# Kernel tuning notes

Hardware: AMD Instinct MI355X
Metric: run time of the kernel (lower is better)

The kernel has to match this reference:

```python
import jax, jax.numpy as jnp
import numpy as np

HEADS = 8
DIM_HEAD = 64
ROT_DIM = DIM_HEAD // 2  # RotaryEmbedding(dim=head_dim//2) rotates first 32 dims of each head
THETA = 10000.0


def _rope_cos_sin(T, dtype):
    # rotary_embedding_torch: freqs = 1/theta**(arange(0,dim,2)/dim), len dim//2,
    # angles repeated interleaved across pairs -> (T, ROT_DIM)
    inv = 1.0 / (THETA ** (jnp.arange(0, ROT_DIM, 2, dtype=jnp.float32) / ROT_DIM))
    ang = jnp.arange(T, dtype=jnp.float32)[:, None] * inv[None, :]      # (T, ROT_DIM/2)
    ang = jnp.repeat(ang, 2, axis=-1)                                   # (T, ROT_DIM) interleaved
    return jnp.cos(ang).astype(dtype), jnp.sin(ang).astype(dtype)


def _rotate_half(x):
    # pairs (x1, x2) -> (-x2, x1), interleaved layout '... (d 2)'
    x = x.reshape(x.shape[:-1] + (-1, 2))
    x = jnp.stack([-x[..., 1], x[..., 0]], axis=-1)
    return x.reshape(x.shape[:-2] + (-1,))


def _apply_rope(x, cos, sin):
    # x: (N, h, T, dh); rotate first ROT_DIM dims, pass through the rest
    xr, xp = x[..., :ROT_DIM], x[..., ROT_DIM:]
    xr = xr * cos[None, None, :, :] + _rotate_half(xr) * sin[None, None, :, :]
    return jnp.concatenate([xr, xp], axis=-1)


def setup_inputs() -> dict:
    key = jax.random.key(0)
    k1, k2, k3 = jax.random.split(key, 3)
    B, T, H, W, D = 2, 32, 32, 32, 512
    inner = HEADS * DIM_HEAD
    x = jax.random.normal(k1, (B, T, H, W, D), dtype=jnp.float32)
    w_qkv = jax.random.normal(k2, (D, 3 * inner), dtype=jnp.float32) * (D ** -0.5)
    w_out = jax.random.normal(k3, (inner, D), dtype=jnp.float32) * (inner ** -0.5)
    b_out = jnp.zeros((D,), dtype=jnp.float32)
    return {"x": x, "w_qkv": w_qkv, "w_out": w_out, "b_out": b_out}


def reference(x, w_qkv, w_out, b_out):
    B, T, H, W, D = x.shape
    qkv = jnp.einsum('bthwd,de->bthwe', x, w_qkv)               # (B,T,H,W,3*inner)
    q, k, v = jnp.split(qkv, 3, axis=-1)

    def to_axial(t):  # (B,T,H,W,inner) -> (B*H*W, heads, T, dh)
        t = t.reshape(B, T, H, W, HEADS, DIM_HEAD)
        t = jnp.transpose(t, (0, 2, 3, 4, 1, 5))
        return t.reshape(B * H * W, HEADS, T, DIM_HEAD)

    q, k, v = to_axial(q), to_axial(k), to_axial(v)
    cos, sin = _rope_cos_sin(T, x.dtype)
    q = _apply_rope(q, cos, sin)
    k = _apply_rope(k, cos, sin)

    scale = DIM_HEAD ** -0.5
    scores = jnp.einsum('nhqd,nhkd->nhqk', q, k) * scale        # (N,h,T,T)
    causal = jnp.tril(jnp.ones((T, T), dtype=bool))
    scores = jnp.where(causal[None, None, :, :], scores, jnp.finfo(scores.dtype).min)
    attn = jax.nn.softmax(scores, axis=-1)
    out = jnp.einsum('nhqk,nhkd->nhqd', attn, v)                # (N,h,T,dh)

    out = out.reshape(B, H, W, HEADS, T, DIM_HEAD)
    out = jnp.transpose(out, (0, 4, 1, 2, 3, 5)).reshape(B, T, H, W, HEADS * DIM_HEAD)
    return jnp.einsum('bthwe,ed->bthwd', out, w_out) + b_out
```

## Files before the change

### kernel.cpp

```cpp
#include <hip/hip_runtime.h>
#include <hip/hip_bf16.h>
#include <math.h>

#define HEADS  8
#define TT     32
#define DMODEL 512
#define HWSZ   1024
#define TSTRIDE (HWSZ*DMODEL)

#define NQKV (3*DMODEL*DMODEL)
#define NOUT (DMODEL*DMODEL)
#define NTAB 512

typedef __attribute__((ext_vector_type(8)))  short bf16x8;
typedef __attribute__((ext_vector_type(16))) float f32x16;
typedef __attribute__((ext_vector_type(4)))  short s16x4;
typedef __attribute__((ext_vector_type(2)))  unsigned int u32x2;

__device__ __forceinline__ unsigned short f2bf(float f) {
    unsigned int u = __builtin_bit_cast(unsigned int, f);
    u += 0x7FFFu + ((u >> 16) & 1u);
    return (unsigned short)(u >> 16);
}

__device__ __forceinline__ unsigned int pk_bf(float a, float b) {
    return (unsigned int)f2bf(a) | ((unsigned int)f2bf(b) << 16);
}

__device__ __forceinline__ f32x16 fz16() {
    f32x16 v = {0.f,0.f,0.f,0.f,0.f,0.f,0.f,0.f,0.f,0.f,0.f,0.f,0.f,0.f,0.f,0.f};
    return v;
}

__global__ __launch_bounds__(256)
void taa_prep(const float* __restrict__ wqkv, const float* __restrict__ wout,
              unsigned short* __restrict__ ws) {
    long i = (long)blockIdx.x * 256 + threadIdx.x;
    unsigned short* wqf = ws;
    unsigned short* wof = ws + NQKV;
    float* cs = (float*)(wof + NOUT);
    float* sn = cs + NTAB;
    if (i < NQKV) {
        int i8 = (int)(i & 7), lane = (int)((i >> 3) & 63), blk = (int)(i >> 9);
        int k05 = blk & 15, t = blk >> 4;
        int n = t * 16 + (lane & 15);
        int k = k05 * 32 + (lane >> 4) * 8 + i8;
        wqf[i] = f2bf(wqkv[(long)k * 1536 + n]);
    } else if (i < NQKV + NOUT) {
        long j = i - NQKV;
        int i8 = (int)(j & 7), lane = (int)((j >> 3) & 63), blk = (int)(j >> 9);
        int k05 = blk & 15, t = blk >> 4;
        int col = t * 16 + (lane & 15);
        int k = k05 * 32 + (lane >> 4) * 8 + i8;
        wof[j] = f2bf(wout[(long)k * 512 + col]);
    } else if (i < NQKV + NOUT + NTAB) {
        int j = (int)(i - NQKV - NOUT);
        int t = j >> 4, f = j & 15;
        float inv = powf(10000.f, -(float)(2 * f) / 32.f);
        float sv, cv;
        sincosf((float)t * inv, &sv, &cv);
        cs[j] = cv; sn[j] = sv;
    }
}

#define X_OFF  0
#define Q_OFF  65536
#define K_OFF  81920
#define V_OFF  98304
#define PV_OFF 114688
#define CS_OFF 131072
#define SN_OFF 133120
#define LDS_SZ 135168

#define XF(g, blk, ln) (X_OFF + ((g) << 15) + ((blk) << 10) + ((((ln) << 4)) ^ (((blk) & 7) << 4)))
#define RS(base, r, cB) ((base) + ((r) << 7) + ((cB) ^ (((r) & 7) << 4)))
#define VS(base, d, cB) ((base) + ((d) << 6) + ((cB) ^ (((d) & 7) << 3)))

#define MFMA16(a, b, c) __builtin_amdgcn_mfma_f32_16x16x32_bf16((a), (b), (c), 0, 0, 0)
#define MFMA32(a, b, c) __builtin_amdgcn_mfma_f32_32x32x16_bf16((a), (b), (c), 0, 0, 0)

__global__ __launch_bounds__(512, 1)
void taa_main(const float* __restrict__ x,
              const unsigned short* __restrict__ ws,
              const float* __restrict__ b_out,
              float* __restrict__ out) {
    extern __shared__ __align__(16) unsigned char smem[];

    const unsigned short* wqf = ws;
    const unsigned short* wof = ws + NQKV;
    const float* cs_gl = (const float*)(wof + NOUT);
    const float* sn_gl = cs_gl + NTAB;

    const int tid  = threadIdx.x;
    const int lane = tid & 63;
    const int wv   = tid >> 6;
    const int quad = lane >> 4;
    const int lid  = lane & 15;

    const int n0 = blockIdx.x * 2;
    const long long base0 = ((long long)(n0 >> 10) * (TT * HWSZ) + (n0 & 1023)) * DMODEL;
    const int n1 = n0 + 1;
    const long long base1 = ((long long)(n1 >> 10) * (TT * HWSZ) + (n1 & 1023)) * DMODEL;

    float* cs_l = (float*)(smem + CS_OFF);
    float* sn_l = (float*)(smem + SN_OFF);
    for (int i = tid; i < NTAB; i += 512) { cs_l[i] = cs_gl[i]; sn_l[i] = sn_gl[i]; }

    for (int idx = tid; idx < 4096; idx += 512) {
        int g  = idx >> 11;
        int r  = (idx >> 6) & 31;
        int c8 = idx & 63;
        long long bg = g ? base1 : base0;
        const float4* src = (const float4*)(x + bg + (long long)r * TSTRIDE + c8 * 8);
        float4 f0 = src[0], f1 = src[1];
        s16x4 lo, hi;
        lo[0] = (short)f2bf(f0.x); lo[1] = (short)f2bf(f0.y);
        lo[2] = (short)f2bf(f0.z); lo[3] = (short)f2bf(f0.w);
        hi[0] = (short)f2bf(f1.x); hi[1] = (short)f2bf(f1.y);
        hi[2] = (short)f2bf(f1.z); hi[3] = (short)f2bf(f1.w);
        int blk = ((r >> 4) << 4) + (c8 >> 2);
        int ln  = ((c8 & 3) << 4) | (r & 15);
        int dest = XF(g, blk, ln);
        *(s16x4*)(smem + dest)     = lo;
        *(s16x4*)(smem + dest + 8) = hi;
    }

    typedef __attribute__((ext_vector_type(4))) float f32x4;
    f32x4 oacc[4][2][2];
    #pragma unroll
    for (int j = 0; j < 4; ++j)
        #pragma unroll
        for (int g = 0; g < 2; ++g)
            #pragma unroll
            for (int mt = 0; mt < 2; ++mt) oacc[j][g][mt] = (f32x4){0.f, 0.f, 0.f, 0.f};

    __syncthreads();

    for (int it = 0; it < 4; ++it) {
        const int hpair = it * 2;

        for (int rnd = 0; rnd < 3; ++rnd) {
            int ct  = rnd * 8 + wv;
            int m   = ct >> 3;
            int hh  = (ct >> 2) & 1;
            int t16 = ct & 3;
            int T   = m * 32 + (hpair + hh) * 4 + t16;
            const unsigned short* wp = wqf + ((long)T * 16) * 512 + lane * 8;
            f32x4 acc[2][2];
            #pragma unroll
            for (int g = 0; g < 2; ++g)
                #pragma unroll
                for (int mt = 0; mt < 2; ++mt) acc[g][mt] = (f32x4){0.f, 0.f, 0.f, 0.f};
            #pragma unroll 4
            for (int k05 = 0; k05 < 16; ++k05) {
                bf16x8 bw = *(const bf16x8*)(wp + (long)k05 * 512);
                #pragma unroll
                for (int g = 0; g < 2; ++g)
                    #pragma unroll
                    for (int mt = 0; mt < 2; ++mt) {
                        bf16x8 a = *(const bf16x8*)(smem + XF(g, mt * 16 + k05, lane));
                        acc[g][mt] = MFMA16(a, bw, acc[g][mt]);
                    }
            }
            if (m < 2) {
                int dstb = ((m == 0) ? Q_OFF : K_OFF) + hh * 4096;
                if (t16 < 2) {
                    #pragma unroll
                    for (int g = 0; g < 2; ++g)
                        #pragma unroll
                        for (int mt = 0; mt < 2; ++mt)
                            #pragma unroll
                            for (int r = 0; r < 4; ++r) {
                                float v = acc[g][mt][r];
                                float p = __shfl_xor(v, 1, 64);
                                int trow = mt * 16 + quad * 4 + r;
                                int colh = t16 * 16 + lid;
                                int jj = colh >> 1;
                                float cv = cs_l[trow * 16 + jj];
                                float sv = sn_l[trow * 16 + jj];
                                float res = (colh & 1) ? (v * cv + p * sv) : (v * cv - p * sv);
                                *(unsigned short*)(smem + RS(dstb + g * 8192, trow, colh * 2)) = f2bf(res);
                            }
                } else {
                    #pragma unroll
                    for (int g = 0; g < 2; ++g)
                        #pragma unroll
                        for (int mt = 0; mt < 2; ++mt)
                            #pragma unroll
                            for (int r = 0; r < 4; ++r) {
                                int trow = mt * 16 + quad * 4 + r;
                                *(unsigned short*)(smem + RS(dstb + g * 8192, trow, (t16 * 16 + lid) * 2)) = f2bf(acc[g][mt][r]);
                            }
                }
            } else {
                #pragma unroll
                for (int g = 0; g < 2; ++g)
                    #pragma unroll
                    for (int mt = 0; mt < 2; ++mt) {
                        int d  = t16 * 16 + lid;
                        int t0 = mt * 16 + quad * 4;
                        s16x4 pk;
                        pk[0] = (short)f2bf(acc[g][mt][0]); pk[1] = (short)f2bf(acc[g][mt][1]);
                        pk[2] = (short)f2bf(acc[g][mt][2]); pk[3] = (short)f2bf(acc[g][mt][3]);
                        *(s16x4*)(smem + VS(V_OFF + (g * 2 + hh) * 4096, d, t0 * 2)) = pk;
                    }
            }
        }
        __syncthreads();

        {
            int g  = wv >> 2;
            int hh = (wv >> 1) & 1;
            int dt = wv & 1;
            int qr  = Q_OFF  + (g * 2 + hh) * 4096;
            int kr  = K_OFF  + (g * 2 + hh) * 4096;
            int vr  = V_OFF  + (g * 2 + hh) * 4096;
            int pvr = PV_OFF + (g * 2 + hh) * 4096;
            int tq = lane & 31;
            int hf = lane >> 5;

            f32x16 sc = fz16();
            #pragma unroll
            for (int j = 0; j < 4; ++j) {
                bf16x8 aK = *(const bf16x8*)(smem + RS(kr, tq, j * 32 + hf * 16));
                bf16x8 bQ = *(const bf16x8*)(smem + RS(qr, tq, j * 32 + hf * 16));
                sc = MFMA32(aK, bQ, sc);
            }
            float pe[16];
            float mx = -1e30f;
            #pragma unroll
            for (int r = 0; r < 16; ++r) {
                int tk = (r & 3) + 8 * (r >> 2) + 4 * hf;
                float v = (tk <= tq) ? sc[r] * 0.125f : -1e30f;
                pe[r] = v;
                mx = fmaxf(mx, v);
            }
            mx = fmaxf(mx, __shfl_xor(mx, 32, 64));
            float sum = 0.f;
            #pragma unroll
            for (int r = 0; r < 16; ++r) {
                float e = __expf(pe[r] - mx);
                pe[r] = e;
                sum += e;
            }
            sum += __shfl_xor(sum, 32, 64);
            float inv = 1.f / sum;
            bf16x8 pa0, pa1;
            #pragma unroll
            for (int i2 = 0; i2 < 8; ++i2) {
                pa0[i2] = (short)f2bf(pe[i2] * inv);
                pa1[i2] = (short)f2bf(pe[8 + i2] * inv);
            }
            int d = dt * 32 + tq;
            f32x16 o = fz16();
            {
                s16x4 lo = *(const s16x4*)(smem + VS(vr, d, 8 * hf));
                s16x4 hi = *(const s16x4*)(smem + VS(vr, d, 16 + 8 * hf));
                bf16x8 bv;
                bv[0] = lo[0]; bv[1] = lo[1]; bv[2] = lo[2]; bv[3] = lo[3];
                bv[4] = hi[0]; bv[5] = hi[1]; bv[6] = hi[2]; bv[7] = hi[3];
                o = MFMA32(bv, pa0, o);
            }
            {
                s16x4 lo = *(const s16x4*)(smem + VS(vr, d, 32 + 8 * hf));
                s16x4 hi = *(const s16x4*)(smem + VS(vr, d, 48 + 8 * hf));
                bf16x8 bv;
                bv[0] = lo[0]; bv[1] = lo[1]; bv[2] = lo[2]; bv[3] = lo[3];
                bv[4] = hi[0]; bv[5] = hi[1]; bv[6] = hi[2]; bv[7] = hi[3];
                o = MFMA32(bv, pa1, o);
            }
            #pragma unroll
            for (int c = 0; c < 4; ++c) {
                u32x2 pk2;
                pk2[0] = pk_bf(o[4 * c + 0], o[4 * c + 1]);
                pk2[1] = pk_bf(o[4 * c + 2], o[4 * c + 3]);
                int db = dt * 32 + c * 8 + 4 * hf;
                *(u32x2*)(smem + RS(pvr, tq, db * 2)) = pk2;
            }
        }
        __syncthreads();

        {
            #pragma unroll
            for (int k05h = 0; k05h < 4; ++k05h) {
                int hh   = k05h >> 1;
                int dblk = k05h & 1;
                int kb   = (hpair + hh) * 2 + dblk;
                bf16x8 a[2][2];
                #pragma unroll
                for (int g = 0; g < 2; ++g)
                    #pragma unroll
                    for (int mt = 0; mt < 2; ++mt)
                        a[g][mt] = *(const bf16x8*)(smem + RS(PV_OFF + (g * 2 + hh) * 4096, lid + 16 * mt, dblk * 64 + quad * 16));
                #pragma unroll
                for (int j = 0; j < 4; ++j) {
                    int ct = wv + 8 * j;
                    bf16x8 bw = *(const bf16x8*)(wof + ((long)(ct * 16 + kb)) * 512 + lane * 8);
                    #pragma unroll
                    for (int g = 0; g < 2; ++g)
                        #pragma unroll
                        for (int mt = 0; mt < 2; ++mt)
                            oacc[j][g][mt] = MFMA16(a[g][mt], bw, oacc[j][g][mt]);
                }
            }
        }
    }

    #pragma unroll
    for (int j = 0; j < 4; ++j) {
        int col = (wv + 8 * j) * 16 + lid;
        float bias = b_out[col];
        #pragma unroll
        for (int g = 0; g < 2; ++g) {
            long long bg = g ? base1 : base0;
            #pragma unroll
            for (int mt = 0; mt < 2; ++mt)
                #pragma unroll
                for (int r = 0; r < 4; ++r) {
                    int t = mt * 16 + quad * 4 + r;
                    out[bg + (long long)t * TSTRIDE + col] = oacc[j][g][mt][r] + bias;
                }
        }
    }
}

extern "C" void kernel_launch(void* const* d_in, const int* in_sizes, int n_in,
                              void* d_out, int out_size, void* d_ws, size_t ws_size,
                              hipStream_t stream) {
    const float* x     = (const float*)d_in[0];
    const float* w_qkv = (const float*)d_in[1];
    const float* w_out = (const float*)d_in[2];
    const float* b_out = (const float*)d_in[3];
    float* out = (float*)d_out;
    (void)in_sizes; (void)n_in; (void)out_size; (void)ws_size;

    unsigned short* ws = (unsigned short*)d_ws;

    taa_prep<<<dim3(4098), dim3(256), 0, stream>>>(w_qkv, w_out, ws);
    taa_main<<<dim3(1024), dim3(512), LDS_SZ, stream>>>(x, ws, b_out, out);
}
```

Baseline: 228.8 us.

## Process one axial sequence per block with 256 threads instead of two

Each block now handles a single (b,h,w) sequence with 4 waves instead of two sequences with 8 waves. This halves LDS use (about 68KB) and drops the launch bound minimum, so two blocks can reside per CU and the grid doubles to 2048. In exchange, each weight tile loaded from global memory is reused across only one sequence instead of two, which doubles weight traffic per output.

```diff
diff --git a/kernel.cpp b/kernel.cpp
--- a/kernel.cpp
+++ b/kernel.cpp
@@ -64,22 +64,22 @@
 }
 
 #define X_OFF  0
-#define Q_OFF  65536
-#define K_OFF  81920
-#define V_OFF  98304
-#define PV_OFF 114688
-#define CS_OFF 131072
-#define SN_OFF 133120
-#define LDS_SZ 135168
-
-#define XF(g, blk, ln) (X_OFF + ((g) << 15) + ((blk) << 10) + ((((ln) << 4)) ^ (((blk) & 7) << 4)))
+#define Q_OFF  32768
+#define K_OFF  40960
+#define V_OFF  49152
+#define PV_OFF 57344
+#define CS_OFF 65536
+#define SN_OFF 67584
+#define LDS_SZ 69632
+
+#define XF(blk, ln) (X_OFF + ((blk) << 10) + ((((ln) << 4)) ^ (((blk) & 7) << 4)))
 #define RS(base, r, cB) ((base) + ((r) << 7) + ((cB) ^ (((r) & 7) << 4)))
 #define VS(base, d, cB) ((base) + ((d) << 6) + ((cB) ^ (((d) & 7) << 3)))
 
 #define MFMA16(a, b, c) __builtin_amdgcn_mfma_f32_16x16x32_bf16((a), (b), (c), 0, 0, 0)
 #define MFMA32(a, b, c) __builtin_amdgcn_mfma_f32_32x32x16_bf16((a), (b), (c), 0, 0, 0)
 
-__global__ __launch_bounds__(512, 1)
+__global__ __launch_bounds__(256)
 void taa_main(const float* __restrict__ x,
               const unsigned short* __restrict__ ws,
               const float* __restrict__ b_out,
@@ -97,21 +97,17 @@
     const int quad = lane >> 4;
     const int lid  = lane & 15;
 
-    const int n0 = blockIdx.x * 2;
-    const long long base0 = ((long long)(n0 >> 10) * (TT * HWSZ) + (n0 & 1023)) * DMODEL;
-    const int n1 = n0 + 1;
-    const long long base1 = ((long long)(n1 >> 10) * (TT * HWSZ) + (n1 & 1023)) * DMODEL;
+    const int n  = blockIdx.x;
+    const long long base = ((long long)(n >> 10) * (TT * HWSZ) + (n & 1023)) * DMODEL;
 
     float* cs_l = (float*)(smem + CS_OFF);
     float* sn_l = (float*)(smem + SN_OFF);
-    for (int i = tid; i < NTAB; i += 512) { cs_l[i] = cs_gl[i]; sn_l[i] = sn_gl[i]; }
-
-    for (int idx = tid; idx < 4096; idx += 512) {
-        int g  = idx >> 11;
-        int r  = (idx >> 6) & 31;
+    for (int i = tid; i < NTAB; i += 256) { cs_l[i] = cs_gl[i]; sn_l[i] = sn_gl[i]; }
+
+    for (int idx = tid; idx < 2048; idx += 256) {
+        int r  = idx >> 6;
         int c8 = idx & 63;
-        long long bg = g ? base1 : base0;
-        const float4* src = (const float4*)(x + bg + (long long)r * TSTRIDE + c8 * 8);
+        const float4* src = (const float4*)(x + base + (long long)r * TSTRIDE + c8 * 8);
         float4 f0 = src[0], f1 = src[1];
         s16x4 lo, hi;
         lo[0] = (short)f2bf(f0.x); lo[1] = (short)f2bf(f0.y);
@@ -120,102 +116,88 @@
         hi[2] = (short)f2bf(f1.z); hi[3] = (short)f2bf(f1.w);
         int blk = ((r >> 4) << 4) + (c8 >> 2);
         int ln  = ((c8 & 3) << 4) | (r & 15);
-        int dest = XF(g, blk, ln);
+        int dest = XF(blk, ln);
         *(s16x4*)(smem + dest)     = lo;
         *(s16x4*)(smem + dest + 8) = hi;
     }
 
     typedef __attribute__((ext_vector_type(4))) float f32x4;
-    f32x4 oacc[4][2][2];
+    f32x4 oacc[8][2];
     #pragma unroll
-    for (int j = 0; j < 4; ++j)
+    for (int j = 0; j < 8; ++j)
         #pragma unroll
-        for (int g = 0; g < 2; ++g)
-            #pragma unroll
-            for (int mt = 0; mt < 2; ++mt) oacc[j][g][mt] = (f32x4){0.f, 0.f, 0.f, 0.f};
+        for (int mt = 0; mt < 2; ++mt) oacc[j][mt] = (f32x4){0.f, 0.f, 0.f, 0.f};
 
     __syncthreads();
 
     for (int it = 0; it < 4; ++it) {
         const int hpair = it * 2;
 
-        for (int rnd = 0; rnd < 3; ++rnd) {
-            int ct  = rnd * 8 + wv;
+        for (int rnd = 0; rnd < 6; ++rnd) {
+            int ct  = rnd * 4 + wv;
             int m   = ct >> 3;
             int hh  = (ct >> 2) & 1;
             int t16 = ct & 3;
             int T   = m * 32 + (hpair + hh) * 4 + t16;
             const unsigned short* wp = wqf + ((long)T * 16) * 512 + lane * 8;
-            f32x4 acc[2][2];
-            #pragma unroll
-            for (int g = 0; g < 2; ++g)
-                #pragma unroll
-                for (int mt = 0; mt < 2; ++mt) acc[g][mt] = (f32x4){0.f, 0.f, 0.f, 0.f};
+            f32x4 acc[2];
+            acc[0] = (f32x4){0.f, 0.f, 0.f, 0.f};
+            acc[1] = (f32x4){0.f, 0.f, 0.f, 0.f};
             #pragma unroll 4
             for (int k05 = 0; k05 < 16; ++k05) {
                 bf16x8 bw = *(const bf16x8*)(wp + (long)k05 * 512);
-                #pragma unroll
-                for (int g = 0; g < 2; ++g)
-                    #pragma unroll
-                    for (int mt = 0; mt < 2; ++mt) {
-                        bf16x8 a = *(const bf16x8*)(smem + XF(g, mt * 16 + k05, lane));
-                        acc[g][mt] = MFMA16(a, bw, acc[g][mt]);
-                    }
+                bf16x8 a0 = *(const bf16x8*)(smem + XF(k05, lane));
+                bf16x8 a1 = *(const bf16x8*)(smem + XF(16 + k05, lane));
+                acc[0] = MFMA16(a0, bw, acc[0]);
+                acc[1] = MFMA16(a1, bw, acc[1]);
             }
             if (m < 2) {
                 int dstb = ((m == 0) ? Q_OFF : K_OFF) + hh * 4096;
                 if (t16 < 2) {
                     #pragma unroll
-                    for (int g = 0; g < 2; ++g)
+                    for (int mt = 0; mt < 2; ++mt)
                         #pragma unroll
-                        for (int mt = 0; mt < 2; ++mt)
-                            #pragma unroll
-                            for (int r = 0; r < 4; ++r) {
-                                float v = acc[g][mt][r];
-                                float p = __shfl_xor(v, 1, 64);
-                                int trow = mt * 16 + quad * 4 + r;
-                                int colh = t16 * 16 + lid;
-                                int jj = colh >> 1;
-                                float cv = cs_l[trow * 16 + jj];
-                                float sv = sn_l[trow * 16 + jj];
-                                float res = (colh & 1) ? (v * cv + p * sv) : (v * cv - p * sv);
-                                *(unsigned short*)(smem + RS(dstb + g * 8192, trow, colh * 2)) = f2bf(res);
-                            }
+                        for (int r = 0; r < 4; ++r) {
+                            float v = acc[mt][r];
+                            float p = __shfl_xor(v, 1, 64);
+                            int trow = mt * 16 + quad * 4 + r;
+                            int colh = t16 * 16 + lid;
+                            int jj = colh >> 1;
+                            float cv = cs_l[trow * 16 + jj];
+                            float sv = sn_l[trow * 16 + jj];
+                            float res = (colh & 1) ? (v * cv + p * sv) : (v * cv - p * sv);
+                            *(unsigned short*)(smem + RS(dstb, trow, colh * 2)) = f2bf(res);
+                        }
                 } else {
                     #pragma unroll
-                    for (int g = 0; g < 2; ++g)
+                    for (int mt = 0; mt < 2; ++mt)
                         #pragma unroll
-                        for (int mt = 0; mt < 2; ++mt)
-                            #pragma unroll
-                            for (int r = 0; r < 4; ++r) {
-                                int trow = mt * 16 + quad * 4 + r;
-                                *(unsigned short*)(smem + RS(dstb + g * 8192, trow, (t16 * 16 + lid) * 2)) = f2bf(acc[g][mt][r]);
-                            }
+                        for (int r = 0; r < 4; ++r) {
+                            int trow = mt * 16 + quad * 4 + r;
+                            *(unsigned short*)(smem + RS(dstb, trow, (t16 * 16 + lid) * 2)) = f2bf(acc[mt][r]);
+                        }
                 }
             } else {
                 #pragma unroll
-                for (int g = 0; g < 2; ++g)
-                    #pragma unroll
-                    for (int mt = 0; mt < 2; ++mt) {
-                        int d  = t16 * 16 + lid;
-                        int t0 = mt * 16 + quad * 4;
-                        s16x4 pk;
-                        pk[0] = (short)f2bf(acc[g][mt][0]); pk[1] = (short)f2bf(acc[g][mt][1]);
-                        pk[2] = (short)f2bf(acc[g][mt][2]); pk[3] = (short)f2bf(acc[g][mt][3]);
-                        *(s16x4*)(smem + VS(V_OFF + (g * 2 + hh) * 4096, d, t0 * 2)) = pk;
-                    }
+                for (int mt = 0; mt < 2; ++mt) {
+                    int d  = t16 * 16 + lid;
+                    int t0 = mt * 16 + quad * 4;
+                    s16x4 pk;
+                    pk[0] = (short)f2bf(acc[mt][0]); pk[1] = (short)f2bf(acc[mt][1]);
+                    pk[2] = (short)f2bf(acc[mt][2]); pk[3] = (short)f2bf(acc[mt][3]);
+                    *(s16x4*)(smem + VS(V_OFF + hh * 4096, d, t0 * 2)) = pk;
+                }
             }
         }
         __syncthreads();
 
         {
-            int g  = wv >> 2;
-            int hh = (wv >> 1) & 1;
+            int hh = wv >> 1;
             int dt = wv & 1;
-            int qr  = Q_OFF  + (g * 2 + hh) * 4096;
-            int kr  = K_OFF  + (g * 2 + hh) * 4096;
-            int vr  = V_OFF  + (g * 2 + hh) * 4096;
-            int pvr = PV_OFF + (g * 2 + hh) * 4096;
+            int qr  = Q_OFF  + hh * 4096;
+            int kr  = K_OFF  + hh * 4096;
+            int vr  = V_OFF  + hh * 4096;
+            int pvr = PV_OFF + hh * 4096;
             int tq = lane & 31;
             int hf = lane >> 5;
 
@@ -286,41 +268,33 @@
                 int hh   = k05h >> 1;
                 int dblk = k05h & 1;
                 int kb   = (hpair + hh) * 2 + dblk;
-                bf16x8 a[2][2];
+                bf16x8 a[2];
                 #pragma unroll
-                for (int g = 0; g < 2; ++g)
+                for (int mt = 0; mt < 2; ++mt)
+                    a[mt] = *(const bf16x8*)(smem + RS(PV_OFF + hh * 4096, lid + 16 * mt, dblk * 64 + quad * 16));
+                #pragma unroll
+                for (int j = 0; j < 8; ++j) {
+                    int ct = wv + 4 * j;
+                    bf16x8 bw = *(const bf16x8*)(wof + ((long)(ct * 16 + kb)) * 512 + lane * 8);
                     #pragma unroll
                     for (int mt = 0; mt < 2; ++mt)
-                        a[g][mt] = *(const bf16x8*)(smem + RS(PV_OFF + (g * 2 + hh) * 4096, lid + 16 * mt, dblk * 64 + quad * 16));
-                #pragma unroll
-                for (int j = 0; j < 4; ++j) {
-                    int ct = wv + 8 * j;
-                    bf16x8 bw = *(const bf16x8*)(wof + ((long)(ct * 16 + kb)) * 512 + lane * 8);
-                    #pragma unroll
-                    for (int g = 0; g < 2; ++g)
-                        #pragma unroll
-                        for (int mt = 0; mt < 2; ++mt)
-                            oacc[j][g][mt] = MFMA16(a[g][mt], bw, oacc[j][g][mt]);
+                        oacc[j][mt] = MFMA16(a[mt], bw, oacc[j][mt]);
                 }
             }
         }
     }
 
     #pragma unroll
-    for (int j = 0; j < 4; ++j) {
-        int col = (wv + 8 * j) * 16 + lid;
+    for (int j = 0; j < 8; ++j) {
+        int col = (wv + 4 * j) * 16 + lid;
         float bias = b_out[col];
         #pragma unroll
-        for (int g = 0; g < 2; ++g) {
-            long long bg = g ? base1 : base0;
-            #pragma unroll
-            for (int mt = 0; mt < 2; ++mt)
-                #pragma unroll
-                for (int r = 0; r < 4; ++r) {
-                    int t = mt * 16 + quad * 4 + r;
-                    out[bg + (long long)t * TSTRIDE + col] = oacc[j][g][mt][r] + bias;
-                }
-        }
+        for (int mt = 0; mt < 2; ++mt)
+            #pragma unroll
+            for (int r = 0; r < 4; ++r) {
+                int t = mt * 16 + quad * 4 + r;
+                out[base + (long long)t * TSTRIDE + col] = oacc[j][mt][r] + bias;
+            }
     }
 }
 
@@ -337,5 +311,5 @@
     unsigned short* ws = (unsigned short*)d_ws;
 
     taa_prep<<<dim3(4098), dim3(256), 0, stream>>>(w_qkv, w_out, ws);
-    taa_main<<<dim3(1024), dim3(512), LDS_SZ, stream>>>(x, ws, b_out, out);
-}
+    taa_main<<<dim3(2048), dim3(256), LDS_SZ, stream>>>(x, ws, b_out, out);
+}
```

Result: slower. 274.0 us (+19.7%).
